# Kernel tuning notes

Hardware: AMD Instinct MI355X
Metric: run time of the kernel (lower is better)

The kernel has to match this reference:

```python
import jax, jax.numpy as jnp
import numpy as np

N_HEAD = 8


def setup_inputs() -> dict:
    key = jax.random.key(0)
    k1, k2, k3, k4 = jax.random.split(key, 4)
    B, C, T, F = 2, 128, 512, 512
    x = jax.random.normal(k1, (B, C, T, F), dtype=jnp.float32)
    Wq = jax.random.normal(k2, (F, F), dtype=jnp.float32) * (F ** -0.5)
    bq = jax.random.normal(k3, (F,), dtype=jnp.float32) * 0.02
    Wk = jax.random.normal(k4, (F, F), dtype=jnp.float32) * (F ** -0.5)
    return {"x": x, "Wq": Wq, "bq": bq, "Wk": Wk}


def reference(x, Wq, bq, Wk):
    B, C, T, F = x.shape
    H = N_HEAD
    d = F // H
    # v: permute (0,1,3,2) -> (B,C,F,T), flatten -> (B,C,F*T)
    v = jnp.transpose(x, (0, 1, 3, 2)).reshape(B, C, F * T)
    # mean over permuted dim 3 (== original T axis)
    xm = jnp.mean(x, axis=2)  # (B,C,F)
    q = xm @ Wq.T + bq        # (B,C,F)
    k = xm @ Wk.T             # (B,C,F)
    scale = d ** (-0.25)
    qh = q.reshape(B, C, H, d).transpose(0, 2, 1, 3) * scale   # (B,H,C,d)
    kh = k.reshape(B, C, H, d).transpose(0, 2, 3, 1) * scale   # (B,H,d,C)
    dv = (F * T) // H
    vh = v.reshape(B, C, H, dv).transpose(0, 2, 1, 3)          # (B,H,C,dv)
    qk = jnp.einsum('bhcd,bhdk->bhck', qh, kh)                 # (B,H,C,C)
    w = jax.nn.softmax(qk.astype(jnp.float32), axis=-1).astype(qh.dtype)
    wv = jnp.einsum('bhck,bhkd->bhcd', w, vh)                  # (B,H,C,dv)
    wv = wv.transpose(0, 2, 1, 3).reshape(B, C, F * T).reshape(B, C, F, T)
    # inverse permute (0,1,3,2) -> (B,C,T,F)
    return jnp.transpose(wv, (0, 1, 3, 2))
```

## Files before the change

kernel.cpp:

```cpp
#include <hip/hip_runtime.h>
#include <hip/hip_bf16.h>

#define CC 128
#define TT 512
#define FF 512
#define CS (TT * FF)

typedef __attribute__((ext_vector_type(8))) short short8;
typedef __attribute__((ext_vector_type(4))) float f32x4;

__device__ __forceinline__ unsigned short f2b(float f) {
    union { float f; unsigned u; } a; a.f = f;
    unsigned r = a.u + 0x7fffu + ((a.u >> 16) & 1u);
    return (unsigned short)(r >> 16);
}

__global__ __launch_bounds__(1024) void mean_kernel(const float* __restrict__ x,
                                                    float* __restrict__ xm) {
    int bc = blockIdx.x;
    int q4  = threadIdx.x & 127;
    int par = threadIdx.x >> 7;
    const float4* xp = (const float4*)(x + (size_t)bc * (TT * FF));
    float4 s0 = make_float4(0.f,0.f,0.f,0.f), s1 = make_float4(0.f,0.f,0.f,0.f);
    float4 s2 = make_float4(0.f,0.f,0.f,0.f), s3 = make_float4(0.f,0.f,0.f,0.f);
    #pragma unroll 4
    for (int k = 0; k < 64; k += 4) {
        float4 a = xp[(par + 8 * k) * 128 + q4];
        float4 b = xp[(par + 8 * (k + 1)) * 128 + q4];
        float4 c = xp[(par + 8 * (k + 2)) * 128 + q4];
        float4 d = xp[(par + 8 * (k + 3)) * 128 + q4];
        s0.x += a.x; s0.y += a.y; s0.z += a.z; s0.w += a.w;
        s1.x += b.x; s1.y += b.y; s1.z += b.z; s1.w += b.w;
        s2.x += c.x; s2.y += c.y; s2.z += c.z; s2.w += c.w;
        s3.x += d.x; s3.y += d.y; s3.z += d.z; s3.w += d.w;
    }
    s0.x += s1.x + s2.x + s3.x; s0.y += s1.y + s2.y + s3.y;
    s0.z += s1.z + s2.z + s3.z; s0.w += s1.w + s2.w + s3.w;
    __shared__ float4 part[1024];
    part[threadIdx.x] = s0;
    __syncthreads();
    if (par == 0) {
        const float inv = 1.0f / (float)TT;
        float4 acc = make_float4(0.f,0.f,0.f,0.f);
        #pragma unroll
        for (int j = 0; j < 8; ++j) {
            float4 v = part[q4 + 128 * j];
            acc.x += v.x; acc.y += v.y; acc.z += v.z; acc.w += v.w;
        }
        acc.x *= inv; acc.y *= inv; acc.z *= inv; acc.w *= inv;
        ((float4*)xm)[bc * 128 + q4] = acc;
    }
}

__global__ void qk_kernel(const float* __restrict__ xm, const float* __restrict__ Wq,
                          const float* __restrict__ bq, const float* __restrict__ Wk,
                          float* __restrict__ qo, float* __restrict__ ko) {
    __shared__ float xs[32][65];
    __shared__ float wqs[32][65];
    __shared__ float wks[32][65];
    int ft = blockIdx.x, rt = blockIdx.y;
    int t = threadIdx.x;
    int tx = t & 15, ty = t >> 4;
    float qa[2][2] = {{0.f,0.f},{0.f,0.f}}, ka[2][2] = {{0.f,0.f},{0.f,0.f}};
    for (int kc = 0; kc < 512; kc += 64) {
        __syncthreads();
        for (int i = t; i < 2048; i += 256) {
            int r = i >> 6, cc2 = i & 63;
            xs[r][cc2]  = xm[(rt * 32 + r) * 512 + kc + cc2];
            wqs[r][cc2] = Wq[(ft * 32 + r) * 512 + kc + cc2];
            wks[r][cc2] = Wk[(ft * 32 + r) * 512 + kc + cc2];
        }
        __syncthreads();
        #pragma unroll 8
        for (int kk = 0; kk < 64; ++kk) {
            float x0 = xs[ty*2][kk],  x1 = xs[ty*2+1][kk];
            float a0 = wqs[tx*2][kk], a1 = wqs[tx*2+1][kk];
            float b0 = wks[tx*2][kk], b1 = wks[tx*2+1][kk];
            qa[0][0] += x0*a0; qa[0][1] += x0*a1;
            qa[1][0] += x1*a0; qa[1][1] += x1*a1;
            ka[0][0] += x0*b0; ka[0][1] += x0*b1;
            ka[1][0] += x1*b0; ka[1][1] += x1*b1;
        }
    }
    #pragma unroll
    for (int i = 0; i < 2; ++i) {
        int r = rt * 32 + ty * 2 + i;
        #pragma unroll
        for (int j = 0; j < 2; ++j) {
            int f = ft * 32 + tx * 2 + j;
            qo[r * 512 + f] = qa[i][j] + bq[f];
            ko[r * 512 + f] = ka[i][j];
        }
    }
}

__global__ void attn_w_kernel(const float* __restrict__ q, const float* __restrict__ k,
                              float* __restrict__ w) {
    int idx = blockIdx.x;
    int bh = idx >> 7, c = idx & 127;
    int b = bh >> 3, h = bh & 7;
    int f0 = h * 64;
    __shared__ float qv[64];
    __shared__ float wmax[2];
    __shared__ float wsum[2];
    int t = threadIdx.x;
    if (t < 64) qv[t] = q[((b * CC + c) * FF) + f0 + t];
    __syncthreads();
    const float* kp = k + ((size_t)(b * CC + t) * FF) + f0;
    float acc = 0.f;
    #pragma unroll
    for (int j = 0; j < 64; j += 4) {
        float4 kv = *(const float4*)(kp + j);
        acc += qv[j] * kv.x + qv[j+1] * kv.y + qv[j+2] * kv.z + qv[j+3] * kv.w;
    }
    float logit = acc * 0.125f;
    float m = logit;
    #pragma unroll
    for (int o = 32; o >= 1; o >>= 1) m = fmaxf(m, __shfl_xor(m, o));
    if ((t & 63) == 0) wmax[t >> 6] = m;
    __syncthreads();
    m = fmaxf(wmax[0], wmax[1]);
    float e = expf(logit - m);
    float s = e;
    #pragma unroll
    for (int o = 32; o >= 1; o >>= 1) s += __shfl_xor(s, o);
    if ((t & 63) == 0) wsum[t >> 6] = s;
    __syncthreads();
    s = wsum[0] + wsum[1];
    w[((size_t)bh * 128 + c) * 128 + t] = e / s;
}

__global__ __launch_bounds__(256, 2) void wv3_kernel(const float* __restrict__ x,
                                                     const float* __restrict__ wmat,
                                                     float* __restrict__ out) {
    int bh = blockIdx.y;
    int b = bh >> 3, h = bh & 7;
    __shared__ unsigned short Wl[128 * 128];

    {
        int tid = threadIdx.x;
        int c = tid & 127, half = tid >> 7;
        const float* wp = wmat + ((size_t)bh * 128 + c) * 128 + half * 64;
        unsigned swz = (unsigned)((c & 7) << 4);
        char* base = (char*)Wl + c * 256;
        #pragma unroll
        for (int j = 0; j < 8; ++j) {
            f32x4 v0 = *(const f32x4*)(wp + j * 8);
            f32x4 v1 = *(const f32x4*)(wp + j * 8 + 4);
            short8 pk;
            pk[0] = (short)f2b(v0[0]); pk[1] = (short)f2b(v0[1]);
            pk[2] = (short)f2b(v0[2]); pk[3] = (short)f2b(v0[3]);
            pk[4] = (short)f2b(v1[0]); pk[5] = (short)f2b(v1[1]);
            pk[6] = (short)f2b(v1[2]); pk[7] = (short)f2b(v1[3]);
            *(short8*)(base + (((unsigned)(half * 128 + j * 16)) ^ swz)) = pk;
        }
    }
    __syncthreads();

    int ln  = threadIdx.x & 63;
    int wq  = threadIdx.x >> 6;
    int l15 = ln & 15;
    int kg  = ln >> 4;
    const float* xb = x + (size_t)b * CC * CS;
    float* ob = out + (size_t)b * CC * CS;

    for (int it = 0; it < 4; ++it) {
        int ti = blockIdx.x * 4 + wq + it * 256;
        int col0 = ti << 5;
        size_t cbase = (size_t)(col0 >> 6) * FF + (h << 6) + (col0 & 63);
        const float* xl = xb + cbase + l15 + (size_t)(kg * 8) * CS;

        f32x4 acc[2][8];
        #pragma unroll
        for (int mt = 0; mt < 2; ++mt)
            #pragma unroll
            for (int ct = 0; ct < 8; ++ct)
                acc[mt][ct] = (f32x4){0.f, 0.f, 0.f, 0.f};

        #pragma unroll
        for (int ks = 0; ks < 4; ++ks) {
            const float* p = xl + (size_t)(ks * 32) * CS;
            float v[8], u[8];
            #pragma unroll
            for (int j = 0; j < 8; ++j) {
                v[j] = p[(size_t)j * CS];
                u[j] = p[(size_t)j * CS + 16];
            }
            short8 a0, a1;
            #pragma unroll
            for (int j = 0; j < 8; ++j) {
                a0[j] = (short)f2b(v[j]);
                a1[j] = (short)f2b(u[j]);
            }
            #pragma unroll
            for (int ct = 0; ct < 8; ++ct) {
                int r = ct * 16 + l15;
                const char* bp = (const char*)Wl + r * 256;
                unsigned sw2 = (unsigned)((r & 7) << 4);
                short8 wf = *(const short8*)(bp + (((unsigned)(ks * 64 + kg * 16)) ^ sw2));
                acc[0][ct] = __builtin_amdgcn_mfma_f32_16x16x32_bf16(a0, wf, acc[0][ct], 0, 0, 0);
                acc[1][ct] = __builtin_amdgcn_mfma_f32_16x16x32_bf16(a1, wf, acc[1][ct], 0, 0, 0);
            }
        }

        float* o0 = ob + cbase + kg * 4;
        #pragma unroll
        for (int ct = 0; ct < 8; ++ct) {
            float* op = o0 + (size_t)(ct * 16 + l15) * CS;
            *(f32x4*)op        = acc[0][ct];
            *(f32x4*)(op + 16) = acc[1][ct];
        }
    }
}

extern "C" void kernel_launch(void* const* d_in, const int* in_sizes, int n_in,
                              void* d_out, int out_size, void* d_ws, size_t ws_size,
                              hipStream_t stream) {
    (void)in_sizes; (void)n_in; (void)out_size; (void)ws_size;
    const float* x  = (const float*)d_in[0];
    const float* Wq = (const float*)d_in[1];
    const float* bq = (const float*)d_in[2];
    const float* Wk = (const float*)d_in[3];
    float* out = (float*)d_out;

    float* ws = (float*)d_ws;
    float* xm = ws;
    float* q  = ws + 131072;
    float* k  = ws + 262144;
    float* w  = ws + 393216;

    hipLaunchKernelGGL(mean_kernel,   dim3(256),    dim3(1024), 0, stream, x, xm);
    hipLaunchKernelGGL(qk_kernel,     dim3(16, 8),  dim3(256),  0, stream, xm, Wq, bq, Wk, q, k);
    hipLaunchKernelGGL(attn_w_kernel, dim3(2048),   dim3(128),  0, stream, q, k, w);
    hipLaunchKernelGGL(wv3_kernel,    dim3(64, 16), dim3(256),  0, stream, x, w, out);
}
```

Measured before the change: 226.7 us.

## Stage x tiles through LDS with coalesced float4 loads and double buffering

Rewrites the weighted-V kernel so each block loads x rows for 8 time steps with coalesced float4 global loads. It converts them to bf16 and transposes them into a double-buffered swizzled LDS tile, then reads MFMA A-fragments from LDS. This replaces the old strided scalar gathers, where each lane loaded single floats across channel planes. The change adds LDS traffic, two barriers per time step and register prefetch of the next tile, and each MFMA pass now covers one 16-wide tile instead of two.

```diff
diff --git a/kernel.cpp b/kernel.cpp
--- a/kernel.cpp
+++ b/kernel.cpp
@@ -8,6 +8,7 @@
 
 typedef __attribute__((ext_vector_type(8))) short short8;
 typedef __attribute__((ext_vector_type(4))) float f32x4;
+typedef __attribute__((ext_vector_type(4))) unsigned short u16x4;
 
 __device__ __forceinline__ unsigned short f2b(float f) {
     union { float f; unsigned u; } a; a.f = f;
@@ -130,15 +131,38 @@
     w[((size_t)bh * 128 + c) * 128 + t] = e / s;
 }
 
-__global__ __launch_bounds__(256, 2) void wv3_kernel(const float* __restrict__ x,
+__global__ __launch_bounds__(256, 2) void wv4_kernel(const float* __restrict__ x,
                                                      const float* __restrict__ wmat,
                                                      float* __restrict__ out) {
-    int bh = blockIdx.y;
+    int bid = blockIdx.x;
+    int bh = bid >> 6;
+    int tg = bid & 63;
     int b = bh >> 3, h = bh & 7;
+
     __shared__ unsigned short Wl[128 * 128];
-
+    __shared__ unsigned short Xt[2][64 * 128];
+
+    int tid = threadIdx.x;
+    const float* xb = x + (size_t)b * CC * CS + (h << 6);
+    float* ob = out + (size_t)b * CC * CS + (h << 6);
+
+    int colg = tid & 15;
+    int cg0  = tid >> 4;
+
+    f32x4 xg[2][4];
     {
-        int tid = threadIdx.x;
+        int t0 = tg * 8;
+        #pragma unroll
+        for (int s = 0; s < 2; ++s) {
+            int cp4 = (cg0 + s * 16) * 4;
+            #pragma unroll
+            for (int jj = 0; jj < 4; ++jj)
+                xg[s][jj] = *(const f32x4*)(xb + (size_t)(cp4 + jj) * CS
+                                               + (size_t)t0 * FF + colg * 4);
+        }
+    }
+
+    {
         int c = tid & 127, half = tid >> 7;
         const float* wp = wmat + ((size_t)bh * 128 + c) * 128 + half * 64;
         unsigned swz = (unsigned)((c & 7) << 4);
@@ -155,61 +179,70 @@
             *(short8*)(base + (((unsigned)(half * 128 + j * 16)) ^ swz)) = pk;
         }
     }
-    __syncthreads();
-
-    int ln  = threadIdx.x & 63;
-    int wq  = threadIdx.x >> 6;
+
+    int ln  = tid & 63;
+    int wq  = tid >> 6;
     int l15 = ln & 15;
     int kg  = ln >> 4;
-    const float* xb = x + (size_t)b * CC * CS;
-    float* ob = out + (size_t)b * CC * CS;
-
-    for (int it = 0; it < 4; ++it) {
-        int ti = blockIdx.x * 4 + wq + it * 256;
-        int col0 = ti << 5;
-        size_t cbase = (size_t)(col0 >> 6) * FF + (h << 6) + (col0 & 63);
-        const float* xl = xb + cbase + l15 + (size_t)(kg * 8) * CS;
-
-        f32x4 acc[2][8];
-        #pragma unroll
-        for (int mt = 0; mt < 2; ++mt)
-            #pragma unroll
-            for (int ct = 0; ct < 8; ++ct)
-                acc[mt][ct] = (f32x4){0.f, 0.f, 0.f, 0.f};
-
+    unsigned xswz = (unsigned)((l15 & 7) << 4);
+
+    for (int ti = 0; ti < 8; ++ti) {
+        int t = tg * 8 + ti;
+        char* xbuf = (char*)Xt[ti & 1];
+
+        #pragma unroll
+        for (int s = 0; s < 2; ++s) {
+            int cp4 = (cg0 + s * 16) * 4;
+            #pragma unroll
+            for (int j = 0; j < 4; ++j) {
+                int col = colg * 4 + j;
+                u16x4 p = { f2b(xg[s][0][j]), f2b(xg[s][1][j]),
+                            f2b(xg[s][2][j]), f2b(xg[s][3][j]) };
+                *(u16x4*)(xbuf + (((unsigned)(col * 256 + cp4 * 2))
+                                  ^ ((unsigned)((col & 7) << 4)))) = p;
+            }
+        }
+        __syncthreads();
+
+        if (ti < 7) {
+            int tn = t + 1;
+            #pragma unroll
+            for (int s = 0; s < 2; ++s) {
+                int cp4 = (cg0 + s * 16) * 4;
+                #pragma unroll
+                for (int jj = 0; jj < 4; ++jj)
+                    xg[s][jj] = *(const f32x4*)(xb + (size_t)(cp4 + jj) * CS
+                                                   + (size_t)tn * FF + colg * 4);
+            }
+        }
+
+        f32x4 acc[8];
+        #pragma unroll
+        for (int ct = 0; ct < 8; ++ct) acc[ct] = (f32x4){0.f, 0.f, 0.f, 0.f};
+
+        int coll = wq * 16 + l15;
+        const char* xrow = xbuf + coll * 256;
         #pragma unroll
         for (int ks = 0; ks < 4; ++ks) {
-            const float* p = xl + (size_t)(ks * 32) * CS;
-            float v[8], u[8];
-            #pragma unroll
-            for (int j = 0; j < 8; ++j) {
-                v[j] = p[(size_t)j * CS];
-                u[j] = p[(size_t)j * CS + 16];
-            }
-            short8 a0, a1;
-            #pragma unroll
-            for (int j = 0; j < 8; ++j) {
-                a0[j] = (short)f2b(v[j]);
-                a1[j] = (short)f2b(u[j]);
-            }
+            short8 af = *(const short8*)(xrow +
+                            (((unsigned)(ks * 64 + kg * 16)) ^ xswz));
             #pragma unroll
             for (int ct = 0; ct < 8; ++ct) {
                 int r = ct * 16 + l15;
                 const char* bp = (const char*)Wl + r * 256;
-                unsigned sw2 = (unsigned)((r & 7) << 4);
-                short8 wf = *(const short8*)(bp + (((unsigned)(ks * 64 + kg * 16)) ^ sw2));
-                acc[0][ct] = __builtin_amdgcn_mfma_f32_16x16x32_bf16(a0, wf, acc[0][ct], 0, 0, 0);
-                acc[1][ct] = __builtin_amdgcn_mfma_f32_16x16x32_bf16(a1, wf, acc[1][ct], 0, 0, 0);
+                short8 wf = *(const short8*)(bp +
+                                (((unsigned)(ks * 64 + kg * 16))
+                                 ^ ((unsigned)((r & 7) << 4))));
+                acc[ct] = __builtin_amdgcn_mfma_f32_16x16x32_bf16(af, wf, acc[ct], 0, 0, 0);
             }
         }
 
-        float* o0 = ob + cbase + kg * 4;
-        #pragma unroll
-        for (int ct = 0; ct < 8; ++ct) {
-            float* op = o0 + (size_t)(ct * 16 + l15) * CS;
-            *(f32x4*)op        = acc[0][ct];
-            *(f32x4*)(op + 16) = acc[1][ct];
-        }
+        float* o0 = ob + (size_t)t * FF + wq * 16 + kg * 4;
+        #pragma unroll
+        for (int ct = 0; ct < 8; ++ct)
+            *(f32x4*)(o0 + (size_t)(ct * 16 + l15) * CS) = acc[ct];
+
+        __syncthreads();
     }
 }
 
@@ -229,8 +262,8 @@
     float* k  = ws + 262144;
     float* w  = ws + 393216;
 
-    hipLaunchKernelGGL(mean_kernel,   dim3(256),    dim3(1024), 0, stream, x, xm);
-    hipLaunchKernelGGL(qk_kernel,     dim3(16, 8),  dim3(256),  0, stream, xm, Wq, bq, Wk, q, k);
-    hipLaunchKernelGGL(attn_w_kernel, dim3(2048),   dim3(128),  0, stream, q, k, w);
-    hipLaunchKernelGGL(wv3_kernel,    dim3(64, 16), dim3(256),  0, stream, x, w, out);
-}
+    hipLaunchKernelGGL(mean_kernel,   dim3(256),   dim3(1024), 0, stream, x, xm);
+    hipLaunchKernelGGL(qk_kernel,     dim3(16, 8), dim3(256),  0, stream, xm, Wq, bq, Wk, q, k);
+    hipLaunchKernelGGL(attn_w_kernel, dim3(2048),  dim3(128),  0, stream, q, k, w);
+    hipLaunchKernelGGL(wv4_kernel,    dim3(1024),  dim3(256),  0, stream, x, w, out);
+}
```

Result: no change. 226.7 us (+0.0%).
